# Optimization experiments

Measured on AMD Instinct MI355X. Metric: run time of the kernel, lower is better.

## Reference

```python
import jax, jax.numpy as jnp
import numpy as np

B, T, D = 2, 2048, 1024
H, HD = 16, 64  # num_heads, key_size

def setup_inputs() -> dict:
    key = jax.random.key(0)
    ks = jax.random.split(key, 5)
    s = 1.0 / np.sqrt(D)  # VarianceScaling(1.0, fan_in) approx
    return {
        "query": jax.random.normal(ks[0], (B, T, D), dtype=jnp.float32),
        "wq": jax.random.normal(ks[1], (D, H * HD), dtype=jnp.float32) * s,
        "bq": jnp.zeros((H * HD,), dtype=jnp.float32),
        "wk": jax.random.normal(ks[2], (D, H * HD), dtype=jnp.float32) * s,
        "bk": jnp.zeros((H * HD,), dtype=jnp.float32),
        "wv": jax.random.normal(ks[3], (D, H * HD), dtype=jnp.float32) * s,
        "bv": jnp.zeros((H * HD,), dtype=jnp.float32),
        "wo": jax.random.normal(ks[4], (H * HD, D), dtype=jnp.float32) * (1.0 / np.sqrt(H * HD)),
        "bo": jnp.zeros((D,), dtype=jnp.float32),
    }

def reference(query, wq, bq, wk, bk, wv, bv, wo, bo):
    b, t, _ = query.shape
    proj = lambda w, bias: (query @ w + bias).reshape(b, t, H, HD)
    q = proj(wq, bq) / np.sqrt(HD).astype(np.float32)  # fixed scaling on queries
    k = proj(wk, bk)
    v = proj(wv, bv)
    logits = jnp.einsum('bthd,bThd->bhtT', q, k)  # [B,H,T,T]
    causal = jnp.tril(jnp.ones((t, t), dtype=logits.dtype))
    logits = logits - 1e10 * (1.0 - causal)
    weights = jax.nn.softmax(logits, axis=-1)
    attn = jnp.einsum('bhtT,bThd->bthd', weights, v)
    attn_vec = attn.reshape(b, t, H * HD)
    return attn_vec @ wo + bo
```

## Files before the change

### kernel.cpp

```cpp
#include <hip/hip_runtime.h>
#include <hip/hip_bf16.h>
#include <stdint.h>
#include <math.h>

typedef short bf16x8 __attribute__((ext_vector_type(8)));
typedef float f32x4 __attribute__((ext_vector_type(4)));
typedef unsigned u32x4v __attribute__((ext_vector_type(4)));
typedef __hip_bfloat16 bf16;

#define MFMA16(a, b, c) __builtin_amdgcn_mfma_f32_16x16x32_bf16((a), (b), (c), 0, 0, 0)

__device__ __forceinline__ void glds16(const void* g, void* l) {
  __builtin_amdgcn_global_load_lds((const __attribute__((address_space(1))) void*)g,
                                   (__attribute__((address_space(3))) void*)l, 16, 0, 0);
}

__device__ __forceinline__ bf16x8 ld8(const bf16* p) {
  return *reinterpret_cast<const bf16x8*>(p);
}

__device__ __forceinline__ void pl32swap(unsigned& a, unsigned& b) {
  asm volatile("v_permlane32_swap_b32 %0, %1" : "+v"(a), "+v"(b));
}
__device__ __forceinline__ void pl16swap(unsigned& a, unsigned& b) {
  asm volatile("v_permlane16_swap_b32 %0, %1" : "+v"(a), "+v"(b));
}


__global__ void k_prep(const float* __restrict__ query,
                       const float* __restrict__ wq, const float* __restrict__ wk,
                       const float* __restrict__ wv, const float* __restrict__ wo,
                       bf16* __restrict__ X, bf16* __restrict__ Wqkvt, bf16* __restrict__ Wot) {
  __shared__ float tile[32][33];
  const int z = blockIdx.z;
  if (z < 4) {
    const float* src = (z == 0) ? wq : (z == 1) ? wk : (z == 2) ? wv : wo;
    bf16* dst = (z < 3) ? (Wqkvt + (size_t)z * 1024 * 1024) : Wot;
    const int tx = threadIdx.x & 31, ty = threadIdx.x >> 5;
    const int x = blockIdx.x * 32 + tx;
    const int y0 = blockIdx.y * 32;
#pragma unroll
    for (int i = 0; i < 4; ++i) tile[ty + i * 8][tx] = src[(size_t)(y0 + ty + i * 8) * 1024 + x];
    __syncthreads();
#pragma unroll
    for (int i = 0; i < 4; ++i) {
      int c = blockIdx.x * 32 + ty + i * 8;
      dst[(size_t)c * 1024 + y0 + tx] = __float2bfloat16(tile[tx][ty + i * 8]);
    }
  } else {
    const int vb = (z - 4) * 1024 + blockIdx.y * 32 + blockIdx.x;
    const int i = vb * 256 + threadIdx.x;
    float4 v = reinterpret_cast<const float4*>(query)[i];
    bf16 a0 = __float2bfloat16(v.x), a1 = __float2bfloat16(v.y);
    bf16 a2 = __float2bfloat16(v.z), a3 = __float2bfloat16(v.w);
    ushort4 r;
    r.x = reinterpret_cast<unsigned short&>(a0);
    r.y = reinterpret_cast<unsigned short&>(a1);
    r.z = reinterpret_cast<unsigned short&>(a2);
    r.w = reinterpret_cast<unsigned short&>(a3);
    reinterpret_cast<ushort4*>(X)[i] = r;
  }
}


__device__ __forceinline__ void gemm_core(const bf16* __restrict__ A, const bf16* __restrict__ Bt,
                                          int K, int arow0, int bcol0,
                                          bf16* As, bf16* Bs, f32x4 acc[4][4]) {
  const int tid = threadIdx.x, lane = tid & 63, w = tid >> 6;
  const int rsub = lane >> 3, slot = lane & 7;
  const int srcslot = slot ^ rsub;
  const int wrow = (w >> 1) * 64, wcol = (w & 1) * 64;
  const int lr = lane & 15, lg = lane >> 4;
  const int nkt = K >> 6;
  for (int kt = 0; kt < nkt; ++kt) {
    const int k0 = kt * 64;
    if (kt) __syncthreads();
#pragma unroll
    for (int i = 0; i < 4; ++i) {
      const int chunk = w * 4 + i;
      glds16(A + (size_t)(arow0 + chunk * 8 + rsub) * K + k0 + srcslot * 8, As + chunk * 512);
      glds16(Bt + (size_t)(bcol0 + chunk * 8 + rsub) * K + k0 + srcslot * 8, Bs + chunk * 512);
    }
    __syncthreads();
#pragma unroll
    for (int kk = 0; kk < 2; ++kk) {
      bf16x8 af[4], bfv[4];
#pragma unroll
      for (int m = 0; m < 4; ++m) {
        const int row = wrow + m * 16 + lr;
        const int byte = (row * 128 + ((kk * 32 + lg * 8) << 1)) ^ ((row & 7) << 4);
        af[m] = *reinterpret_cast<const bf16x8*>(reinterpret_cast<const char*>(As) + byte);
      }
#pragma unroll
      for (int n = 0; n < 4; ++n) {
        const int row = wcol + n * 16 + lr;
        const int byte = (row * 128 + ((kk * 32 + lg * 8) << 1)) ^ ((row & 7) << 4);
        bfv[n] = *reinterpret_cast<const bf16x8*>(reinterpret_cast<const char*>(Bs) + byte);
      }
#pragma unroll
      for (int m = 0; m < 4; ++m)
#pragma unroll
        for (int n = 0; n < 4; ++n) acc[m][n] = MFMA16(af[m], bfv[n], acc[m][n]);
    }
  }
}


__global__ __launch_bounds__(256) void k_gemm_qkv(
    const bf16* __restrict__ X, const bf16* __restrict__ Wt,
    const float* __restrict__ bq, const float* __restrict__ bk, const float* __restrict__ bv,
    bf16* __restrict__ Qo, bf16* __restrict__ Ko, bf16* __restrict__ Vt) {
  __shared__ bf16 As[128 * 64], Bs[128 * 64];
  f32x4 acc[4][4];
#pragma unroll
  for (int i = 0; i < 4; ++i)
#pragma unroll
    for (int j = 0; j < 4; ++j) acc[i][j] = (f32x4){0.f, 0.f, 0.f, 0.f};
  const int arow0 = blockIdx.y * 128, bcol0 = blockIdx.x * 128;
  gemm_core(X, Wt, 1024, arow0, bcol0, As, Bs, acc);
  const int lane = threadIdx.x & 63, w = threadIdx.x >> 6;
  const int wrow = (w >> 1) * 64, wcol = (w & 1) * 64;
  const int lr = lane & 15, lg = lane >> 4;
  const float QSCALE = 0.125f * 1.4426950408889634f;
#pragma unroll
  for (int mi = 0; mi < 4; ++mi) {
#pragma unroll
    for (int ni = 0; ni < 4; ++ni) {
      const int r0 = arow0 + wrow + mi * 16 + lg * 4;
      const int col = bcol0 + wcol + ni * 16 + lr;
      const int which = col >> 10, cw = col & 1023, h = cw >> 6, hd = cw & 63;
      const int b = r0 >> 11, t0 = r0 & 2047;
      if (which == 2) {
        const float bias = bv[cw];
        ushort4 pk;
#pragma unroll
        for (int j = 0; j < 4; ++j) {
          bf16 hv = __float2bfloat16(acc[mi][ni][j] + bias);
          reinterpret_cast<unsigned short*>(&pk)[j] = reinterpret_cast<unsigned short&>(hv);
        }
        *reinterpret_cast<ushort4*>(Vt + ((size_t)((b * 16 + h) * 64 + hd)) * 2048 + t0) = pk;
      } else {
        const float bias = which ? bk[cw] : bq[cw];
        const float scale = which ? 1.0f : QSCALE;
        bf16* dst = which ? Ko : Qo;
#pragma unroll
        for (int j = 0; j < 4; ++j) {
          float v = (acc[mi][ni][j] + bias) * scale;
          dst[((size_t)((b * 16 + h) * 2048) + t0 + j) * 64 + hd] = __float2bfloat16(v);
        }
      }
    }
  }
}


__global__ __launch_bounds__(256) void k_attn(const bf16* __restrict__ Q, const bf16* __restrict__ Kc,
                                              const bf16* __restrict__ Vt, bf16* __restrict__ attn,
                                              float* __restrict__ Opart, float* __restrict__ Lpart) {
  __shared__ bf16 Ks[2][64 * 64];
  __shared__ bf16 Vs[2][64 * 64];
  const int lane = threadIdx.x & 63, w = threadIdx.x >> 6;
  const int lr = lane & 15, lg = lane >> 4;
  const int rsub = lane >> 3, slot = lane & 7;
  const int srcslot = slot ^ rsub;
  const int bh = blockIdx.x;
  const int y = blockIdx.y;
  int qt, ch;
  if (y < 32) { qt = 31 - (y >> 1); ch = y & 1; }
  else        { qt = 47 - y;        ch = 0; }
  const bool split = (qt >= 16);
  const int it0 = ch * 16;
  const int it1 = (split && ch == 0) ? 16 : (qt + 1);
  const int b = bh >> 4, h = bh & 15;
  const bf16* Qp = Q + (size_t)bh * 2048 * 64;
  const bf16* Kp = Kc + (size_t)bh * 2048 * 64;
  const bf16* Vp = Vt + (size_t)bh * 64 * 2048;

  const int q0 = qt * 64 + w * 16;
  const bf16x8 qa0 = ld8(Qp + (size_t)(q0 + lr) * 64 + lg * 8);
  const bf16x8 qa1 = ld8(Qp + (size_t)(q0 + lr) * 64 + 32 + lg * 8);
  f32x4 o[4];
#pragma unroll
  for (int n = 0; n < 4; ++n) o[n] = (f32x4){0.f, 0.f, 0.f, 0.f};
  float l_ = 0.f;
  const float MBIAS = -8.0f * 1.4426950408889634f;
  const f32x4 minit = {MBIAS, MBIAS, MBIAS, MBIAS};

#pragma unroll
  for (int i = 0; i < 2; ++i) {
    const int ck = w * 2 + i;
    glds16(Kp + (size_t)(it0 * 64 + ck * 8 + rsub) * 64 + srcslot * 8, &Ks[0][ck * 512]);
    glds16(Vp + (size_t)(ck * 8 + rsub) * 2048 + it0 * 64 + srcslot * 8, &Vs[0][ck * 512]);
  }
  __syncthreads();
  int cur = 0;

#pragma unroll 1
  for (int it = it0; it < it1; ++it) {
    if (it + 1 < it1) {
#pragma unroll
      for (int i = 0; i < 2; ++i) {
        const int ck = w * 2 + i;
        glds16(Kp + (size_t)((it + 1) * 64 + ck * 8 + rsub) * 64 + srcslot * 8, &Ks[cur ^ 1][ck * 512]);
        glds16(Vp + (size_t)(ck * 8 + rsub) * 2048 + (it + 1) * 64 + srcslot * 8, &Vs[cur ^ 1][ck * 512]);
      }
    }
    f32x4 s[4];
    const char* Kb = reinterpret_cast<const char*>(&Ks[cur][0]);
#pragma unroll
    for (int n = 0; n < 4; ++n) {
      const int row = n * 16 + lr;
      const int rsw = (row & 7) << 4;
      bf16x8 kb0 = *reinterpret_cast<const bf16x8*>(Kb + ((row * 128 + lg * 16) ^ rsw));
      bf16x8 kb1 = *reinterpret_cast<const bf16x8*>(Kb + ((row * 128 + 64 + lg * 16) ^ rsw));
      s[n] = MFMA16(kb0, qa0, minit);
      s[n] = MFMA16(kb1, qa1, s[n]);
    }
    if (it == qt) {
      const int qme = q0 + lr - it * 64 - lg * 4;
#pragma unroll
      for (int n = 0; n < 4; ++n)
#pragma unroll
        for (int j = 0; j < 4; ++j)
          if (n * 16 + j > qme) s[n][j] = -1e30f;
    }
    float p[4][4];
#pragma unroll
    for (int n = 0; n < 4; ++n)
#pragma unroll
      for (int j = 0; j < 4; ++j) {
        p[n][j] = __builtin_amdgcn_exp2f(s[n][j]);
        l_ += p[n][j];
      }
    unsigned pw[4][2];
#pragma unroll
    for (int n = 0; n < 4; ++n) {
      pw[n][0] = __builtin_amdgcn_perm(__float_as_uint(p[n][1]), __float_as_uint(p[n][0]), 0x07060302u);
      pw[n][1] = __builtin_amdgcn_perm(__float_as_uint(p[n][3]), __float_as_uint(p[n][2]), 0x07060302u);
    }
#pragma unroll
    for (int n1 = 0; n1 < 2; ++n1)
#pragma unroll
      for (int hh = 0; hh < 2; ++hh) {
        pl32swap(pw[2 * n1][hh], pw[2 * n1 + 1][hh]);
        pl16swap(pw[2 * n1][hh], pw[2 * n1 + 1][hh]);
      }
    bf16x8 pa[2];
#pragma unroll
    for (int n1 = 0; n1 < 2; ++n1) {
      u32x4v tv = (u32x4v){pw[2 * n1][0], pw[2 * n1][1], pw[2 * n1 + 1][0], pw[2 * n1 + 1][1]};
      pa[n1] = __builtin_bit_cast(bf16x8, tv);
    }
    const char* Vb = reinterpret_cast<const char*>(&Vs[cur][0]);
#pragma unroll
    for (int n2 = 0; n2 < 4; ++n2) {
#pragma unroll
      for (int kc = 0; kc < 2; ++kc) {
        const int row = n2 * 16 + lr;
        const int rsw = (row & 7) << 4;
        bf16x8 vb = *reinterpret_cast<const bf16x8*>(Vb + ((row * 128 + (kc * 32 + lg * 8) * 2) ^ rsw));
        o[n2] = MFMA16(pa[kc], vb, o[n2]);
      }
    }
    __syncthreads();
    cur ^= 1;
  }
  l_ += __shfl_xor(l_, 16);
  l_ += __shfl_xor(l_, 32);
  if (split) {
    const int sl = ((bh * 16 + (qt - 16)) * 2 + ch);
    float* Op = Opart + (size_t)sl * 4096;
#pragma unroll
    for (int j = 0; j < 4; ++j) {
      const int ql = w * 16 + lg * 4 + j;
#pragma unroll
      for (int n2 = 0; n2 < 4; ++n2) Op[ql * 64 + n2 * 16 + lr] = o[n2][j];
    }
    if (lane < 16) Lpart[sl * 64 + w * 16 + lr] = l_;
  } else {
#pragma unroll
    for (int j = 0; j < 4; ++j) {
      const float inv = 1.0f / __shfl(l_, lg * 4 + j);
      const int qq = q0 + lg * 4 + j;
#pragma unroll
      for (int n2 = 0; n2 < 4; ++n2)
        attn[((size_t)(b * 2048 + qq)) * 1024 + h * 64 + n2 * 16 + lr] = __float2bfloat16(o[n2][j] * inv);
    }
  }
}

__global__ __launch_bounds__(256) void k_attn_combine(const float* __restrict__ Opart,
                                                      const float* __restrict__ Lpart,
                                                      bf16* __restrict__ attn) {
  __shared__ float Ls[64];
  const int bh = blockIdx.x, qt = 16 + blockIdx.y;
  const int b = bh >> 4, h = bh & 15;
  const int sl0 = (bh * 16 + (qt - 16)) * 2;
  const int tid = threadIdx.x;
  if (tid < 64) Ls[tid] = Lpart[sl0 * 64 + tid] + Lpart[(sl0 + 1) * 64 + tid];
  __syncthreads();
  const float4* O0 = reinterpret_cast<const float4*>(Opart + (size_t)sl0 * 4096);
  const float4* O1 = reinterpret_cast<const float4*>(Opart + (size_t)(sl0 + 1) * 4096);
#pragma unroll
  for (int k = 0; k < 4; ++k) {
    const int e4 = tid + k * 256;
    const int q = e4 >> 4, d0 = (e4 & 15) * 4;
    float4 a = O0[e4], c = O1[e4];
    const float inv = 1.0f / Ls[q];
    ushort4 r;
    bf16 v0 = __float2bfloat16((a.x + c.x) * inv);
    bf16 v1 = __float2bfloat16((a.y + c.y) * inv);
    bf16 v2 = __float2bfloat16((a.z + c.z) * inv);
    bf16 v3 = __float2bfloat16((a.w + c.w) * inv);
    r.x = reinterpret_cast<unsigned short&>(v0);
    r.y = reinterpret_cast<unsigned short&>(v1);
    r.z = reinterpret_cast<unsigned short&>(v2);
    r.w = reinterpret_cast<unsigned short&>(v3);
    *reinterpret_cast<ushort4*>(attn + ((size_t)(b * 2048 + qt * 64 + q)) * 1024 + h * 64 + d0) = r;
  }
}


__global__ __launch_bounds__(256) void k_gemm_out(const bf16* __restrict__ A, const bf16* __restrict__ Wot,
                                                  const float* __restrict__ bo, float* __restrict__ out) {
  __shared__ bf16 As[64 * 64], Bs[128 * 64];
  f32x4 acc[4][2];
#pragma unroll
  for (int i = 0; i < 4; ++i)
#pragma unroll
    for (int j = 0; j < 2; ++j) acc[i][j] = (f32x4){0.f, 0.f, 0.f, 0.f};
  const int arow0 = blockIdx.y * 64, bcol0 = blockIdx.x * 128;
  const int lane = threadIdx.x & 63, w = threadIdx.x >> 6;
  const int rsub = lane >> 3, slot = lane & 7;
  const int srcslot = slot ^ rsub;
  const int lr = lane & 15, lg = lane >> 4;
  for (int kt = 0; kt < 16; ++kt) {
    const int k0 = kt * 64;
    if (kt) __syncthreads();
#pragma unroll
    for (int i = 0; i < 2; ++i) {
      const int chunk = w * 2 + i;
      glds16(A + (size_t)(arow0 + chunk * 8 + rsub) * 1024 + k0 + srcslot * 8, As + chunk * 512);
    }
#pragma unroll
    for (int i = 0; i < 4; ++i) {
      const int chunk = w * 4 + i;
      glds16(Wot + (size_t)(bcol0 + chunk * 8 + rsub) * 1024 + k0 + srcslot * 8, Bs + chunk * 512);
    }
    __syncthreads();
#pragma unroll
    for (int kk = 0; kk < 2; ++kk) {
      bf16x8 af[4], bfv[2];
#pragma unroll
      for (int m = 0; m < 4; ++m) {
        const int row = m * 16 + lr;
        const int byte = (row * 128 + ((kk * 32 + lg * 8) << 1)) ^ ((row & 7) << 4);
        af[m] = *reinterpret_cast<const bf16x8*>(reinterpret_cast<const char*>(As) + byte);
      }
#pragma unroll
      for (int n = 0; n < 2; ++n) {
        const int row = w * 32 + n * 16 + lr;
        const int byte = (row * 128 + ((kk * 32 + lg * 8) << 1)) ^ ((row & 7) << 4);
        bfv[n] = *reinterpret_cast<const bf16x8*>(reinterpret_cast<const char*>(Bs) + byte);
      }
#pragma unroll
      for (int m = 0; m < 4; ++m)
#pragma unroll
        for (int n = 0; n < 2; ++n) acc[m][n] = MFMA16(af[m], bfv[n], acc[m][n]);
    }
  }
#pragma unroll
  for (int mi = 0; mi < 4; ++mi) {
#pragma unroll
    for (int ni = 0; ni < 2; ++ni) {
      const int r0 = arow0 + mi * 16 + lg * 4;
      const int col = bcol0 + w * 32 + ni * 16 + lr;
      const float bias = bo[col];
#pragma unroll
      for (int j = 0; j < 4; ++j) out[(size_t)(r0 + j) * 1024 + col] = acc[mi][ni][j] + bias;
    }
  }
}


extern "C" void kernel_launch(void* const* d_in, const int* in_sizes, int n_in,
                              void* d_out, int out_size, void* d_ws, size_t ws_size,
                              hipStream_t stream) {
  const float* query = (const float*)d_in[0];
  const float* wq = (const float*)d_in[1];
  const float* bq = (const float*)d_in[2];
  const float* wk = (const float*)d_in[3];
  const float* bk = (const float*)d_in[4];
  const float* wv = (const float*)d_in[5];
  const float* bv = (const float*)d_in[6];
  const float* wo = (const float*)d_in[7];
  const float* bo = (const float*)d_in[8];
  float* out = (float*)d_out;
  char* ws = (char*)d_ws;
  const size_t MB = 1u << 20;
  bf16* X     = (bf16*)(ws + 0);
  bf16* Wqkvt = (bf16*)(ws + 8 * MB);
  bf16* Wot   = (bf16*)(ws + 14 * MB);
  bf16* Qb    = (bf16*)(ws + 16 * MB);
  bf16* Kb    = (bf16*)(ws + 24 * MB);
  bf16* Vt    = (bf16*)(ws + 32 * MB);
  bf16* attn  = (bf16*)(ws + 40 * MB);
  float* Opart = (float*)(ws + 48 * MB);
  float* Lpart = (float*)(ws + 64 * MB);

  k_prep<<<dim3(32, 32, 8), 256, 0, stream>>>(query, wq, wk, wv, wo, X, Wqkvt, Wot);
  k_gemm_qkv<<<dim3(24, 32), 256, 0, stream>>>(X, Wqkvt, bq, bk, bv, Qb, Kb, Vt);
  k_attn<<<dim3(32, 48), 256, 0, stream>>>(Qb, Kb, Vt, attn, Opart, Lpart);
  k_attn_combine<<<dim3(32, 16), 256, 0, stream>>>(Opart, Lpart, attn);
  k_gemm_out<<<dim3(8, 64), 256, 0, stream>>>(attn, Wot, bo, out);
}
```

Measured before the change: 98.77 us.

## Use 128-row query tiles in attention with per-wave 2-row-block K/V reuse

Each attention block now handles 128 query rows instead of 64, with each wave owning two 16-row MFMA blocks. Every K/V tile staged in LDS is therefore reused across twice as many queries, halving the grid and the redundant K/V traffic. The row-sum is now computed with an MFMA against a ones vector rather than scalar adds and shuffles. Fully masked 16-row sub-blocks and tiles are skipped, and a constant lookup table handles the new split and scheduling of work across blocks. The cost is more registers per wave and fewer blocks, which may reduce occupancy and load balance.

```diff
diff --git a/kernel.cpp b/kernel.cpp
--- a/kernel.cpp
+++ b/kernel.cpp
@@ -25,6 +25,11 @@
 __device__ __forceinline__ void pl16swap(unsigned& a, unsigned& b) {
   asm volatile("v_permlane16_swap_b32 %0, %1" : "+v"(a), "+v"(b));
 }
+
+__device__ __constant__ unsigned char QTM[24] = {8, 9, 10, 11, 12, 13, 14, 15, 7, 15, 14, 6,
+                                                 13, 5, 12, 4, 11, 3, 10, 2, 9, 1, 8, 0};
+__device__ __constant__ unsigned char CHM[24] = {0, 0, 0, 0, 0, 0, 0, 0, 2, 1, 1, 2,
+                                                 1, 2, 1, 2, 1, 2, 1, 2, 1, 2, 1, 2};
 
 
 __global__ void k_prep(const float* __restrict__ query,
@@ -165,26 +170,33 @@
   const int srcslot = slot ^ rsub;
   const int bh = blockIdx.x;
   const int y = blockIdx.y;
-  int qt, ch;
-  if (y < 32) { qt = 31 - (y >> 1); ch = y & 1; }
-  else        { qt = 47 - y;        ch = 0; }
-  const bool split = (qt >= 16);
-  const int it0 = ch * 16;
-  const int it1 = (split && ch == 0) ? 16 : (qt + 1);
+  const int qt = QTM[y], ch = CHM[y];
+  const int it0 = (ch == 1) ? 16 : 0;
+  const int it1 = (ch == 0) ? 16 : (2 * qt + 2);
   const int b = bh >> 4, h = bh & 15;
   const bf16* Qp = Q + (size_t)bh * 2048 * 64;
   const bf16* Kp = Kc + (size_t)bh * 2048 * 64;
   const bf16* Vp = Vt + (size_t)bh * 64 * 2048;
 
-  const int q0 = qt * 64 + w * 16;
-  const bf16x8 qa0 = ld8(Qp + (size_t)(q0 + lr) * 64 + lg * 8);
-  const bf16x8 qa1 = ld8(Qp + (size_t)(q0 + lr) * 64 + 32 + lg * 8);
-  f32x4 o[4];
-#pragma unroll
-  for (int n = 0; n < 4; ++n) o[n] = (f32x4){0.f, 0.f, 0.f, 0.f};
-  float l_ = 0.f;
+  const int q0 = qt * 128 + w * 32;
+  bf16x8 qa[2][2];
+#pragma unroll
+  for (int m = 0; m < 2; ++m) {
+    qa[m][0] = ld8(Qp + (size_t)(q0 + m * 16 + lr) * 64 + lg * 8);
+    qa[m][1] = ld8(Qp + (size_t)(q0 + m * 16 + lr) * 64 + 32 + lg * 8);
+  }
+  f32x4 o[2][4], ol[2];
+#pragma unroll
+  for (int m = 0; m < 2; ++m) {
+    ol[m] = (f32x4){0.f, 0.f, 0.f, 0.f};
+#pragma unroll
+    for (int n = 0; n < 4; ++n) o[m][n] = (f32x4){0.f, 0.f, 0.f, 0.f};
+  }
   const float MBIAS = -8.0f * 1.4426950408889634f;
   const f32x4 minit = {MBIAS, MBIAS, MBIAS, MBIAS};
+  const short one_bf = (short)0x3F80;
+  const bf16x8 ones = {one_bf, one_bf, one_bf, one_bf, one_bf, one_bf, one_bf, one_bf};
+  const bf16x8 zf = {0, 0, 0, 0, 0, 0, 0, 0};
 
 #pragma unroll
   for (int i = 0; i < 2; ++i) {
@@ -197,6 +209,7 @@
 
 #pragma unroll 1
   for (int it = it0; it < it1; ++it) {
+    const int kv0 = it * 64;
     if (it + 1 < it1) {
 #pragma unroll
       for (int i = 0; i < 2; ++i) {
@@ -205,86 +218,107 @@
         glds16(Vp + (size_t)(ck * 8 + rsub) * 2048 + (it + 1) * 64 + srcslot * 8, &Vs[cur ^ 1][ck * 512]);
       }
     }
-    f32x4 s[4];
-    const char* Kb = reinterpret_cast<const char*>(&Ks[cur][0]);
-#pragma unroll
-    for (int n = 0; n < 4; ++n) {
-      const int row = n * 16 + lr;
-      const int rsw = (row & 7) << 4;
-      bf16x8 kb0 = *reinterpret_cast<const bf16x8*>(Kb + ((row * 128 + lg * 16) ^ rsw));
-      bf16x8 kb1 = *reinterpret_cast<const bf16x8*>(Kb + ((row * 128 + 64 + lg * 16) ^ rsw));
-      s[n] = MFMA16(kb0, qa0, minit);
-      s[n] = MFMA16(kb1, qa1, s[n]);
-    }
-    if (it == qt) {
-      const int qme = q0 + lr - it * 64 - lg * 4;
-#pragma unroll
-      for (int n = 0; n < 4; ++n)
-#pragma unroll
-        for (int j = 0; j < 4; ++j)
-          if (n * 16 + j > qme) s[n][j] = -1e30f;
-    }
-    float p[4][4];
-#pragma unroll
-    for (int n = 0; n < 4; ++n)
-#pragma unroll
-      for (int j = 0; j < 4; ++j) {
-        p[n][j] = __builtin_amdgcn_exp2f(s[n][j]);
-        l_ += p[n][j];
-      }
-    unsigned pw[4][2];
-#pragma unroll
-    for (int n = 0; n < 4; ++n) {
-      pw[n][0] = __builtin_amdgcn_perm(__float_as_uint(p[n][1]), __float_as_uint(p[n][0]), 0x07060302u);
-      pw[n][1] = __builtin_amdgcn_perm(__float_as_uint(p[n][3]), __float_as_uint(p[n][2]), 0x07060302u);
-    }
-#pragma unroll
-    for (int n1 = 0; n1 < 2; ++n1)
-#pragma unroll
-      for (int hh = 0; hh < 2; ++hh) {
-        pl32swap(pw[2 * n1][hh], pw[2 * n1 + 1][hh]);
-        pl16swap(pw[2 * n1][hh], pw[2 * n1 + 1][hh]);
-      }
-    bf16x8 pa[2];
-#pragma unroll
-    for (int n1 = 0; n1 < 2; ++n1) {
-      u32x4v tv = (u32x4v){pw[2 * n1][0], pw[2 * n1][1], pw[2 * n1 + 1][0], pw[2 * n1 + 1][1]};
-      pa[n1] = __builtin_bit_cast(bf16x8, tv);
-    }
-    const char* Vb = reinterpret_cast<const char*>(&Vs[cur][0]);
-#pragma unroll
-    for (int n2 = 0; n2 < 4; ++n2) {
-#pragma unroll
-      for (int kc = 0; kc < 2; ++kc) {
+    if (kv0 <= q0 + 47) {
+      bf16x8 kf0[4], kf1[4];
+      const char* Kb = reinterpret_cast<const char*>(&Ks[cur][0]);
+#pragma unroll
+      for (int n = 0; n < 4; ++n) {
+        const int row = n * 16 + lr;
+        const int rsw = (row & 7) << 4;
+        kf0[n] = *reinterpret_cast<const bf16x8*>(Kb + ((row * 128 + lg * 16) ^ rsw));
+        kf1[n] = *reinterpret_cast<const bf16x8*>(Kb + ((row * 128 + 64 + lg * 16) ^ rsw));
+      }
+      bf16x8 pa[2][2];
+#pragma unroll
+      for (int m = 0; m < 2; ++m) {
+        const int qm0 = q0 + m * 16;
+        if (kv0 > qm0 + 15) {
+          pa[m][0] = zf;
+          pa[m][1] = zf;
+          continue;
+        }
+        f32x4 s[4];
+#pragma unroll
+        for (int n = 0; n < 4; ++n) {
+          s[n] = MFMA16(kf0[n], qa[m][0], minit);
+          s[n] = MFMA16(kf1[n], qa[m][1], s[n]);
+        }
+        if (kv0 + 63 > qm0) {
+          const int qme = qm0 + lr - kv0 - lg * 4;
+#pragma unroll
+          for (int n = 0; n < 4; ++n)
+#pragma unroll
+            for (int j = 0; j < 4; ++j)
+              if (n * 16 + j > qme) s[n][j] = -1e30f;
+        }
+        float p[4][4];
+#pragma unroll
+        for (int n = 0; n < 4; ++n)
+#pragma unroll
+          for (int j = 0; j < 4; ++j) p[n][j] = __builtin_amdgcn_exp2f(s[n][j]);
+        unsigned pw[4][2];
+#pragma unroll
+        for (int n = 0; n < 4; ++n) {
+          pw[n][0] = __builtin_amdgcn_perm(__float_as_uint(p[n][1]), __float_as_uint(p[n][0]), 0x07060302u);
+          pw[n][1] = __builtin_amdgcn_perm(__float_as_uint(p[n][3]), __float_as_uint(p[n][2]), 0x07060302u);
+        }
+#pragma unroll
+        for (int n1 = 0; n1 < 2; ++n1)
+#pragma unroll
+          for (int hh = 0; hh < 2; ++hh) {
+            pl32swap(pw[2 * n1][hh], pw[2 * n1 + 1][hh]);
+            pl16swap(pw[2 * n1][hh], pw[2 * n1 + 1][hh]);
+          }
+#pragma unroll
+        for (int n1 = 0; n1 < 2; ++n1) {
+          u32x4v tv = (u32x4v){pw[2 * n1][0], pw[2 * n1][1], pw[2 * n1 + 1][0], pw[2 * n1 + 1][1]};
+          pa[m][n1] = __builtin_bit_cast(bf16x8, tv);
+        }
+        ol[m] = MFMA16(pa[m][0], ones, ol[m]);
+        ol[m] = MFMA16(pa[m][1], ones, ol[m]);
+      }
+      const char* Vb = reinterpret_cast<const char*>(&Vs[cur][0]);
+#pragma unroll
+      for (int n2 = 0; n2 < 4; ++n2) {
         const int row = n2 * 16 + lr;
         const int rsw = (row & 7) << 4;
-        bf16x8 vb = *reinterpret_cast<const bf16x8*>(Vb + ((row * 128 + (kc * 32 + lg * 8) * 2) ^ rsw));
-        o[n2] = MFMA16(pa[kc], vb, o[n2]);
+#pragma unroll
+        for (int kc = 0; kc < 2; ++kc) {
+          bf16x8 vb = *reinterpret_cast<const bf16x8*>(Vb + ((row * 128 + (kc * 32 + lg * 8) * 2) ^ rsw));
+#pragma unroll
+          for (int m = 0; m < 2; ++m) o[m][n2] = MFMA16(pa[m][kc], vb, o[m][n2]);
+        }
       }
     }
     __syncthreads();
     cur ^= 1;
   }
-  l_ += __shfl_xor(l_, 16);
-  l_ += __shfl_xor(l_, 32);
-  if (split) {
-    const int sl = ((bh * 16 + (qt - 16)) * 2 + ch);
-    float* Op = Opart + (size_t)sl * 4096;
-#pragma unroll
-    for (int j = 0; j < 4; ++j) {
-      const int ql = w * 16 + lg * 4 + j;
-#pragma unroll
-      for (int n2 = 0; n2 < 4; ++n2) Op[ql * 64 + n2 * 16 + lr] = o[n2][j];
-    }
-    if (lane < 16) Lpart[sl * 64 + w * 16 + lr] = l_;
+
+  if (ch != 2) {
+    const int sl = (bh * 8 + (qt - 8)) * 2 + ch;
+    float* Op = Opart + (size_t)sl * 8192;
+#pragma unroll
+    for (int m = 0; m < 2; ++m) {
+#pragma unroll
+      for (int j = 0; j < 4; ++j) {
+        const int ql = w * 32 + m * 16 + lg * 4 + j;
+#pragma unroll
+        for (int n2 = 0; n2 < 4; ++n2) Op[ql * 64 + n2 * 16 + lr] = o[m][n2][j];
+        if (lr == 0) Lpart[sl * 128 + ql] = ol[m][j];
+      }
+    }
   } else {
 #pragma unroll
-    for (int j = 0; j < 4; ++j) {
-      const float inv = 1.0f / __shfl(l_, lg * 4 + j);
-      const int qq = q0 + lg * 4 + j;
-#pragma unroll
-      for (int n2 = 0; n2 < 4; ++n2)
-        attn[((size_t)(b * 2048 + qq)) * 1024 + h * 64 + n2 * 16 + lr] = __float2bfloat16(o[n2][j] * inv);
+    for (int m = 0; m < 2; ++m) {
+#pragma unroll
+      for (int j = 0; j < 4; ++j) {
+        const float inv = 1.0f / ol[m][j];
+        const int qq = q0 + m * 16 + lg * 4 + j;
+#pragma unroll
+        for (int n2 = 0; n2 < 4; ++n2)
+          attn[((size_t)(b * 2048 + qq)) * 1024 + h * 64 + n2 * 16 + lr] =
+              __float2bfloat16(o[m][n2][j] * inv);
+      }
     }
   }
 }
@@ -292,17 +326,17 @@
 __global__ __launch_bounds__(256) void k_attn_combine(const float* __restrict__ Opart,
                                                       const float* __restrict__ Lpart,
                                                       bf16* __restrict__ attn) {
-  __shared__ float Ls[64];
-  const int bh = blockIdx.x, qt = 16 + blockIdx.y;
+  __shared__ float Ls[128];
+  const int bh = blockIdx.x, qt = 8 + blockIdx.y;
   const int b = bh >> 4, h = bh & 15;
-  const int sl0 = (bh * 16 + (qt - 16)) * 2;
+  const int sl0 = (bh * 8 + (qt - 8)) * 2;
   const int tid = threadIdx.x;
-  if (tid < 64) Ls[tid] = Lpart[sl0 * 64 + tid] + Lpart[(sl0 + 1) * 64 + tid];
+  if (tid < 128) Ls[tid] = Lpart[sl0 * 128 + tid] + Lpart[(sl0 + 1) * 128 + tid];
   __syncthreads();
-  const float4* O0 = reinterpret_cast<const float4*>(Opart + (size_t)sl0 * 4096);
-  const float4* O1 = reinterpret_cast<const float4*>(Opart + (size_t)(sl0 + 1) * 4096);
-#pragma unroll
-  for (int k = 0; k < 4; ++k) {
+  const float4* O0 = reinterpret_cast<const float4*>(Opart + (size_t)sl0 * 8192);
+  const float4* O1 = reinterpret_cast<const float4*>(Opart + (size_t)(sl0 + 1) * 8192);
+#pragma unroll
+  for (int k = 0; k < 8; ++k) {
     const int e4 = tid + k * 256;
     const int q = e4 >> 4, d0 = (e4 & 15) * 4;
     float4 a = O0[e4], c = O1[e4];
@@ -316,7 +350,7 @@
     r.y = reinterpret_cast<unsigned short&>(v1);
     r.z = reinterpret_cast<unsigned short&>(v2);
     r.w = reinterpret_cast<unsigned short&>(v3);
-    *reinterpret_cast<ushort4*>(attn + ((size_t)(b * 2048 + qt * 64 + q)) * 1024 + h * 64 + d0) = r;
+    *reinterpret_cast<ushort4*>(attn + ((size_t)(b * 2048 + qt * 128 + q)) * 1024 + h * 64 + d0) = r;
   }
 }
 
@@ -410,7 +444,7 @@
 
   k_prep<<<dim3(32, 32, 8), 256, 0, stream>>>(query, wq, wk, wv, wo, X, Wqkvt, Wot);
   k_gemm_qkv<<<dim3(24, 32), 256, 0, stream>>>(X, Wqkvt, bq, bk, bv, Qb, Kb, Vt);
-  k_attn<<<dim3(32, 48), 256, 0, stream>>>(Qb, Kb, Vt, attn, Opart, Lpart);
-  k_attn_combine<<<dim3(32, 16), 256, 0, stream>>>(Opart, Lpart, attn);
+  k_attn<<<dim3(32, 24), 256, 0, stream>>>(Qb, Kb, Vt, attn, Opart, Lpart);
+  k_attn_combine<<<dim3(32, 8), 256, 0, stream>>>(Opart, Lpart, attn);
   k_gemm_out<<<dim3(8, 64), 256, 0, stream>>>(attn, Wot, bo, out);
 }
```

Result: slower. 104.7 us (+6.0%).
